# Optimization experiments

Hardware: AMD Instinct MI355X
Metric: run time of the kernel (lower is better)

The kernel has to match this reference:

```python
import jax, jax.numpy as jnp
import numpy as np

MAX_ITER = 16
TOL = 1e-3


def setup_inputs() -> dict:
    key = jax.random.key(0)
    k0, k1, k2, k3 = jax.random.split(key, 4)
    B, A, Bd, Y = 16384, 1024, 2, 128
    AT = jax.random.uniform(k0, (B, A), dtype=jnp.float32)
    K = jax.random.uniform(k1, (A, Bd), dtype=jnp.float32)
    BT = jnp.ones((Bd,), dtype=jnp.float32)  # fixed to [1, 1] in the module
    u = jax.random.uniform(k2, (A * Bd, Y), dtype=jnp.float32)
    b = jax.random.uniform(k3, (Y,), dtype=jnp.float32)
    return {"AT": AT, "K": K, "BT": BT, "u": u, "b": b}


def reference(AT, K, BT, u, b):
    batch = AT.shape[0]
    Kp = K ** 2  # 'reparam' constraint

    # Fixed-point matrix-balancing loop (torch.no_grad block) -> constants.
    Ksg = jax.lax.stop_gradient(Kp)
    ATsg = jax.lax.stop_gradient(AT)
    A_dim, B_dim = Kp.shape
    af0 = jnp.zeros((batch, A_dim), jnp.float32)
    bf0 = jnp.zeros((batch, B_dim), jnp.float32)

    def cond(carry):
        _, _, err, i = carry
        return (i < MAX_ITER) & (err >= TOL)

    def body(carry):
        af, bf, _, i = carry
        af_n = ATsg / (bf @ Ksg.T + 1.0)   # (batch, A_dim)
        bf_n = BT / (af_n @ Ksg + 1.0)     # (batch, B_dim)
        err = jnp.max(jnp.abs(af_n - af)) + jnp.max(jnp.abs(bf_n - bf))
        return af_n, bf_n, err, i + 1

    _, bf, _, _ = jax.lax.while_loop(
        cond, body, (af0, bf0, jnp.array(jnp.inf, jnp.float32), 0)
    )
    bf = jax.lax.stop_gradient(bf)

    # Final differentiable iteration.
    af = AT / (bf @ Kp.T + 1.0)            # (batch, A_dim)
    bf = BT / (af @ Kp + 1.0)              # (batch, B_dim)

    # C = K * (AF @ BF^T): rank-1 outer product per batch element.
    C = (Kp[None, :, :] * af[:, :, None] * bf[:, None, :]).reshape(batch, -1)
    return C @ u + b
```

## Files before the change

kernel.cpp:

```cpp
#include <hip/hip_runtime.h>

__device__ __forceinline__ unsigned short f2b(float f) {
    unsigned int u = __builtin_bit_cast(unsigned int, f);
    u += 0x7fffu + ((u >> 16) & 1u);
    return (unsigned short)(u >> 16);
}
__device__ __forceinline__ float fastrcp(float x) {
    return __builtin_amdgcn_rcpf(x);
}
__device__ __forceinline__ unsigned int cvt_pk_bf16(float lo, float hi) {
    unsigned int r;
    asm("v_cvt_pk_bf16_f32 %0, %1, %2" : "=v"(r) : "v"(lo), "v"(hi));
    return r;
}
template<int CTRL>
__device__ __forceinline__ float dpp_add(float x) {
    int s = __builtin_amdgcn_update_dpp(0, __builtin_bit_cast(int, x), CTRL, 0xf, 0xf, true);
    return x + __builtin_bit_cast(float, s);
}
__device__ __forceinline__ float wave_sum_bcast(float x) {
    x = dpp_add<0x111>(x);
    x = dpp_add<0x112>(x);
    x = dpp_add<0x114>(x);
    x = dpp_add<0x118>(x);
    x = dpp_add<0x142>(x);
    x = dpp_add<0x143>(x);
    return __builtin_bit_cast(float,
        __builtin_amdgcn_readlane(__builtin_bit_cast(int, x), 63));
}

typedef short bf16x8_t __attribute__((ext_vector_type(8)));
typedef float f32x4_t  __attribute__((ext_vector_type(4)));

#define NB   16384
#define AD   1024
#define YD   128

__global__ __launch_bounds__(256) void vt_kernel(
    const float* __restrict__ Kq,
    const float* __restrict__ U,
    unsigned short* __restrict__ Vtf)
{
    int o  = blockIdx.x * 256 + threadIdx.x;
    int T  = o >> 14;
    int CQ = (o >> 7) & 127;
    int rr = (o >> 3) & 15;
    int e  = o & 7;
    int n  = T * 16 + rr;
    int a  = CQ * 8 + e;
    int j  = n >> 7;
    int y  = n & 127;
    float k  = Kq[2 * a + j];
    float uv = U[(size_t)(2 * a + j) * YD + y];
    Vtf[o] = f2b(k * k * uv);
}

__global__ __launch_bounds__(512, 4) void fused_kernel(
    const float* __restrict__ AT,
    const float* __restrict__ Kq,
    const float* __restrict__ BTv,
    const unsigned short* __restrict__ Vtf,
    const float* __restrict__ bias,
    float* __restrict__ out)
{
    __shared__ __align__(16) unsigned short lA[16 * 1024];
    __shared__ float lbf[16][2];

    const int t    = threadIdx.x;
    const int lane = t & 63;
    const int w    = t >> 6;
    const int mtile = blockIdx.x;

    float kp0[16], kp1[16];
#pragma unroll
    for (int c = 0; c < 4; ++c) {
        int base = c * 256 + lane * 4;
        float4 k0v = *(const float4*)(Kq + 2 * base);
        float4 k1v = *(const float4*)(Kq + 2 * base + 4);
        kp0[c * 4 + 0] = k0v.x * k0v.x; kp1[c * 4 + 0] = k0v.y * k0v.y;
        kp0[c * 4 + 1] = k0v.z * k0v.z; kp1[c * 4 + 1] = k0v.w * k0v.w;
        kp0[c * 4 + 2] = k1v.x * k1v.x; kp1[c * 4 + 2] = k1v.y * k1v.y;
        kp0[c * 4 + 3] = k1v.z * k1v.z; kp1[c * 4 + 3] = k1v.w * k1v.w;
    }
    const float bt0 = BTv[0], bt1 = BTv[1];

    const float* atb = AT + (size_t)(mtile * 16 + w * 2) * AD;

    float ta[2][16];
#pragma unroll
    for (int r = 0; r < 2; ++r) {
#pragma unroll
        for (int c = 0; c < 4; ++c) {
            float4 av = *(const float4*)(atb + (size_t)r * AD + c * 256 + lane * 4);
            ta[r][c * 4 + 0] = av.x; ta[r][c * 4 + 1] = av.y;
            ta[r][c * 4 + 2] = av.z; ta[r][c * 4 + 3] = av.w;
        }
    }

#pragma unroll
    for (int r = 0; r < 2; ++r) {
        float M[9];
#pragma unroll
        for (int i2 = 0; i2 < 9; ++i2) M[i2] = 0.f;
#pragma unroll
        for (int e = 0; e < 16; ++e) {
            float tv = ta[r][e], p = kp0[e], q2 = kp1[e];
            float u0 = tv * p, u1 = tv * q2;
            M[0] += u0; M[1] += u1;
            float u00 = u0 * p, u01 = u0 * q2, u11 = u1 * q2;
            M[2] += u00; M[3] += u01; M[4] += u11;
            M[5] += u00 * p; M[6] += u00 * q2; M[7] += u01 * q2; M[8] += u11 * q2;
        }
#pragma unroll
        for (int i2 = 0; i2 < 9; ++i2) M[i2] = wave_sum_bcast(M[i2]);

        float bf0 = 0.f, bf1 = 0.f;
#pragma unroll
        for (int it = 0; it < 8; ++it) {
            float q00 = bf0 * bf0, q01 = bf0 * bf1, q11 = bf1 * bf1;
            float s0 = M[0] - (bf0 * M[2] + bf1 * M[3]) + (q00 * M[5] + 2.f * q01 * M[6] + q11 * M[7]);
            float s1 = M[1] - (bf0 * M[3] + bf1 * M[4]) + (q00 * M[6] + 2.f * q01 * M[7] + q11 * M[8]);
            bf0 = bt0 * fastrcp(1.f + s0);
            bf1 = bt1 * fastrcp(1.f + s1);
        }
        const int m = w * 2 + r;
        if (lane == 0) { lbf[m][0] = bf0; lbf[m][1] = bf1; }

#pragma unroll
        for (int c = 0; c < 4; ++c) {
            float v[4];
#pragma unroll
            for (int e = 0; e < 4; ++e) {
                int idx = c * 4 + e;
                v[e] = ta[r][idx] * fastrcp(1.f + bf0 * kp0[idx] + bf1 * kp1[idx]);
            }
            uint2 pk;
            pk.x = cvt_pk_bf16(v[0], v[1]);
            pk.y = cvt_pk_bf16(v[2], v[3]);
            int cg = c * 4 + (lane >> 4);
            int cl = (lane >> 1) & 7;
            int off = (m * 128 + cg * 8 + (cl ^ (m & 7))) * 8 + (lane & 1) * 4;
            *(uint2*)(&lA[off]) = pk;
        }
    }

    __syncthreads();

    const int rr = lane & 15;
    const int hb = lane >> 4;
    const int rx = rr & 7;

    const unsigned short* pB = Vtf + (size_t)w * 16384 + hb * 128 + rr * 8;

    f32x4_t acc[2];
#pragma unroll
    for (int j = 0; j < 2; ++j) acc[j] = (f32x4_t){0.f, 0.f, 0.f, 0.f};

    bf16x8_t fbA[2], fbB[2];

    auto loadB = [&](bf16x8_t* fb, int k0, int kk) {
        int ke = k0 * 16 + kk * 512;
        fb[0] = *(const bf16x8_t*)(pB + ke);
        fb[1] = *(const bf16x8_t*)(pB + ke + 131072);
    };
    auto compute = [&](const bf16x8_t* fb, int k0, int kk) {
        const int cq = kk * 4 + hb;
        bf16x8_t fa = *(const bf16x8_t*)(
            &lA[((rr * 128) + (k0 >> 6) * 8 + (cq ^ rx)) * 8]);
#pragma unroll
        for (int j = 0; j < 2; ++j)
            acc[j] = __builtin_amdgcn_mfma_f32_16x16x32_bf16(fa, fb[j], acc[j], 0, 0, 0);
    };

    loadB(fbA, 0, 0);
    loadB(fbB, 0, 1);
#pragma unroll 1
    for (int k0 = 0; k0 < AD; k0 += 64) {
        __builtin_amdgcn_s_setprio(1);
        compute(fbA, k0, 0);
        __builtin_amdgcn_s_setprio(0);
        if (k0 + 64 < AD) loadB(fbA, k0 + 64, 0);
        __builtin_amdgcn_s_setprio(1);
        compute(fbB, k0, 1);
        __builtin_amdgcn_s_setprio(0);
        if (k0 + 64 < AD) loadB(fbB, k0 + 64, 1);
    }

    const int mloc  = hb * 4;
    const int mbase = mtile * 16 + mloc;
    float2 bfv[4];
#pragma unroll
    for (int r = 0; r < 4; ++r)
        bfv[r] = *(const float2*)(&lbf[mloc + r][0]);
    const int y = w * 16 + rr;
    const float bv = bias[y];
#pragma unroll
    for (int r = 0; r < 4; ++r) {
        float val = bfv[r].x * acc[0][r] + bfv[r].y * acc[1][r] + bv;
        out[(size_t)(mbase + r) * YD + y] = val;
    }
}

extern "C" void kernel_launch(void* const* d_in, const int* in_sizes, int n_in,
                              void* d_out, int out_size, void* d_ws, size_t ws_size,
                              hipStream_t stream) {
    const float* AT  = (const float*)d_in[0];
    const float* Kq  = (const float*)d_in[1];
    const float* BTv = (const float*)d_in[2];
    const float* U   = (const float*)d_in[3];
    const float* bia = (const float*)d_in[4];
    float* out = (float*)d_out;

    unsigned short* Vtf = (unsigned short*)d_ws;

    vt_kernel<<<dim3(1024), dim3(256), 0, stream>>>(Kq, U, Vtf);
    fused_kernel<<<dim3(NB / 16), dim3(512), 0, stream>>>(AT, Kq, BTv, Vtf, bia, out);
}
```

Baseline: 121.9 us.

## Split fused kernel into row-balancing and GEMM kernels with 32-row tiles

Splits the fused kernel into a row kernel, which computes the balancing factors and writes bf16 af tiles in a pre-swizzled layout to workspace, and a separate GEMM kernel. The GEMM kernel loads 32-row A tiles straight into LDS with global_load_lds and runs a 2x2 MFMA accumulator tile, which halves how often each block re-streams Vtf. The cost is an extra 32 MB round trip through global memory for the af tiles, one more kernel launch, and double the LDS per GEMM block.

```diff
diff --git a/kernel.cpp b/kernel.cpp
--- a/kernel.cpp
+++ b/kernel.cpp
@@ -31,6 +31,9 @@
 
 typedef short bf16x8_t __attribute__((ext_vector_type(8)));
 typedef float f32x4_t  __attribute__((ext_vector_type(4)));
+
+#define LDS_PTR(p) ((__attribute__((address_space(3))) void*)(p))
+#define GLB_PTR(p) ((const __attribute__((address_space(1))) void*)(p))
 
 #define NB   16384
 #define AD   1024
@@ -55,21 +58,17 @@
     Vtf[o] = f2b(k * k * uv);
 }
 
-__global__ __launch_bounds__(512, 4) void fused_kernel(
+__global__ __launch_bounds__(512, 4) void row_kernel(
     const float* __restrict__ AT,
     const float* __restrict__ Kq,
     const float* __restrict__ BTv,
-    const unsigned short* __restrict__ Vtf,
-    const float* __restrict__ bias,
-    float* __restrict__ out)
+    unsigned short* __restrict__ afb,
+    float* __restrict__ bff)
 {
-    __shared__ __align__(16) unsigned short lA[16 * 1024];
-    __shared__ float lbf[16][2];
-
     const int t    = threadIdx.x;
     const int lane = t & 63;
     const int w    = t >> 6;
-    const int mtile = blockIdx.x;
+    const int R0   = blockIdx.x * 16 + w * 2;
 
     float kp0[16], kp1[16];
 #pragma unroll
@@ -84,7 +83,7 @@
     }
     const float bt0 = BTv[0], bt1 = BTv[1];
 
-    const float* atb = AT + (size_t)(mtile * 16 + w * 2) * AD;
+    const float* atb = AT + (size_t)R0 * AD;
 
     float ta[2][16];
 #pragma unroll
@@ -123,9 +122,11 @@
             bf0 = bt0 * fastrcp(1.f + s0);
             bf1 = bt1 * fastrcp(1.f + s1);
         }
-        const int m = w * 2 + r;
-        if (lane == 0) { lbf[m][0] = bf0; lbf[m][1] = bf1; }
-
+        const int R = R0 + r;
+        if (lane == 0) { bff[(size_t)R * 2] = bf0; bff[(size_t)R * 2 + 1] = bf1; }
+
+        unsigned short* base = afb + (size_t)(R >> 5) * 32768 + (size_t)(R & 31) * 1024;
+        const int s7 = R & 7;
 #pragma unroll
         for (int c = 0; c < 4; ++c) {
             float v[4];
@@ -139,11 +140,32 @@
             pk.y = cvt_pk_bf16(v[2], v[3]);
             int cg = c * 4 + (lane >> 4);
             int cl = (lane >> 1) & 7;
-            int off = (m * 128 + cg * 8 + (cl ^ (m & 7))) * 8 + (lane & 1) * 4;
-            *(uint2*)(&lA[off]) = pk;
-        }
-    }
-
+            int off = (cg * 8 + (cl ^ s7)) * 8 + (lane & 1) * 4;
+            *(uint2*)(base + off) = pk;
+        }
+    }
+}
+
+__global__ __launch_bounds__(512, 4) void gemm_kernel(
+    const unsigned short* __restrict__ afb,
+    const unsigned short* __restrict__ Vtf,
+    const float* __restrict__ bff,
+    const float* __restrict__ bias,
+    float* __restrict__ out)
+{
+    __shared__ __align__(16) unsigned short lA[32 * 1024];
+
+    const int t    = threadIdx.x;
+    const int lane = t & 63;
+    const int w    = t >> 6;
+    const int mtile = blockIdx.x;
+
+    const unsigned short* img = afb + (size_t)mtile * 32768;
+#pragma unroll
+    for (int i = 0; i < 8; ++i) {
+        int s = i * 512 + t;
+        __builtin_amdgcn_global_load_lds(GLB_PTR(img + s * 8), LDS_PTR(&lA[s * 8]), 16, 0, 0);
+    }
     __syncthreads();
 
     const int rr = lane & 15;
@@ -152,9 +174,11 @@
 
     const unsigned short* pB = Vtf + (size_t)w * 16384 + hb * 128 + rr * 8;
 
-    f32x4_t acc[2];
-#pragma unroll
-    for (int j = 0; j < 2; ++j) acc[j] = (f32x4_t){0.f, 0.f, 0.f, 0.f};
+    f32x4_t acc[2][2];
+#pragma unroll
+    for (int i = 0; i < 2; ++i)
+#pragma unroll
+        for (int j = 0; j < 2; ++j) acc[i][j] = (f32x4_t){0.f, 0.f, 0.f, 0.f};
 
     bf16x8_t fbA[2], fbB[2];
 
@@ -165,11 +189,16 @@
     };
     auto compute = [&](const bf16x8_t* fb, int k0, int kk) {
         const int cq = kk * 4 + hb;
-        bf16x8_t fa = *(const bf16x8_t*)(
-            &lA[((rr * 128) + (k0 >> 6) * 8 + (cq ^ rx)) * 8]);
-#pragma unroll
-        for (int j = 0; j < 2; ++j)
-            acc[j] = __builtin_amdgcn_mfma_f32_16x16x32_bf16(fa, fb[j], acc[j], 0, 0, 0);
+        bf16x8_t fa[2];
+#pragma unroll
+        for (int i = 0; i < 2; ++i)
+            fa[i] = *(const bf16x8_t*)(
+                &lA[(((i * 16 + rr) * 128) + (k0 >> 6) * 8 + (cq ^ rx)) * 8]);
+#pragma unroll
+        for (int i = 0; i < 2; ++i)
+#pragma unroll
+            for (int j = 0; j < 2; ++j)
+                acc[i][j] = __builtin_amdgcn_mfma_f32_16x16x32_bf16(fa[i], fb[j], acc[i][j], 0, 0, 0);
     };
 
     loadB(fbA, 0, 0);
@@ -186,18 +215,20 @@
         if (k0 + 64 < AD) loadB(fbB, k0 + 64, 1);
     }
 
-    const int mloc  = hb * 4;
-    const int mbase = mtile * 16 + mloc;
-    float2 bfv[4];
-#pragma unroll
-    for (int r = 0; r < 4; ++r)
-        bfv[r] = *(const float2*)(&lbf[mloc + r][0]);
-    const int y = w * 16 + rr;
+    const int y  = w * 16 + rr;
     const float bv = bias[y];
 #pragma unroll
-    for (int r = 0; r < 4; ++r) {
-        float val = bfv[r].x * acc[0][r] + bfv[r].y * acc[1][r] + bv;
-        out[(size_t)(mbase + r) * YD + y] = val;
+    for (int i = 0; i < 2; ++i) {
+        int mbase = mtile * 32 + i * 16 + hb * 4;
+        float2 bfv[4];
+#pragma unroll
+        for (int r = 0; r < 4; ++r)
+            bfv[r] = *(const float2*)(bff + (size_t)(mbase + r) * 2);
+#pragma unroll
+        for (int r = 0; r < 4; ++r) {
+            float val = bfv[r].x * acc[i][0][r] + bfv[r].y * acc[i][1][r] + bv;
+            out[(size_t)(mbase + r) * YD + y] = val;
+        }
     }
 }
 
@@ -211,8 +242,12 @@
     const float* bia = (const float*)d_in[4];
     float* out = (float*)d_out;
 
-    unsigned short* Vtf = (unsigned short*)d_ws;
-
-    vt_kernel<<<dim3(1024), dim3(256), 0, stream>>>(Kq, U, Vtf);
-    fused_kernel<<<dim3(NB / 16), dim3(512), 0, stream>>>(AT, Kq, BTv, Vtf, bia, out);
-}
+    char* ws = (char*)d_ws;
+    unsigned short* Vtf = (unsigned short*)ws;
+    unsigned short* afb = (unsigned short*)(ws + 524288);
+    float*          bff = (float*)(ws + 524288 + 33554432);
+
+    vt_kernel <<<dim3(1024), dim3(256), 0, stream>>>(Kq, U, Vtf);
+    row_kernel <<<dim3(NB / 16), dim3(512), 0, stream>>>(AT, Kq, BTv, afb, bff);
+    gemm_kernel<<<dim3(NB / 32), dim3(512), 0, stream>>>(afb, Vtf, bff, bia, out);
+}
```

After: 126.0 us. 1.03x slower.
